# Performance work log

Measured on AMD Instinct MI355X. Metric: run time of the kernel, lower is better.

## Reference

```python
import jax, jax.numpy as jnp
import numpy as np

IN_F = 4096
OUT_F = 4096
B, S = 4, 2048
BITS = 4
N_LEVELS = 1 << BITS  # 16


def setup_inputs() -> dict:
    key = jax.random.key(0)
    kx, kr, ks, kb = jax.random.split(key, 4)
    x = jax.random.normal(kx, (B, S, IN_F), dtype=jnp.float32)
    # random orthogonal rotation (TurboQuantMSE rotation matrix, seeded)
    g = jax.random.normal(kr, (IN_F, IN_F), dtype=jnp.float32)
    rotation, _ = jnp.linalg.qr(g)
    # 4-bit scalar codebook: Lloyd-Max-style Gaussian levels, scaled for
    # unit-norm rows whose rotated entries ~ N(0, 1/in_features)
    p = (jnp.arange(N_LEVELS, dtype=jnp.float32) + 0.5) / N_LEVELS
    levels = jnp.sqrt(2.0) * jax.scipy.special.erfinv(2.0 * p - 1.0)
    codebook = (levels / jnp.sqrt(jnp.float32(IN_F))).astype(jnp.float32)
    weight_indices = jax.random.randint(jax.random.fold_in(key, 1), (OUT_F, IN_F), 0, N_LEVELS, dtype=jnp.int32)
    weight_scale = jax.random.uniform(ks, (OUT_F,), dtype=jnp.float32, minval=0.5, maxval=2.0)
    bias = jax.random.normal(kb, (OUT_F,), dtype=jnp.float32)
    return {"x": x, "weight_indices": weight_indices, "weight_scale": weight_scale,
            "bias": bias, "rotation": rotation, "codebook": codebook}


def reference(x, weight_indices, weight_scale, bias, rotation, codebook):
    # dequantize: codebook lookup -> inverse rotation -> per-row rescale
    w_rot = codebook[weight_indices]                      # (out, in)
    w_hat = jnp.einsum('oi,ji->oj', w_rot, rotation)      # apply R^T: (out, in)
    w = w_hat * weight_scale[:, None]                     # (out, in)
    # F.linear: x @ W^T + b
    return jnp.einsum('bsi,oi->bso', x, w) + bias
```

## Files before the change

kernel.cpp:

```cpp
#include <hip/hip_runtime.h>

typedef short short8 __attribute__((ext_vector_type(8)));
typedef float f32x4 __attribute__((ext_vector_type(4)));

#define GLOBAL_AS __attribute__((address_space(1)))
#define LDS_AS    __attribute__((address_space(3)))

__device__ __forceinline__ unsigned short f2bf(float f) {
    unsigned u = __builtin_bit_cast(unsigned, f);
    u += 0x7fffu + ((u >> 16) & 1u);
    return (unsigned short)(u >> 16);
}

__global__ __launch_bounds__(256) void k_idx2bf(const int* __restrict__ idx,
                                                const float* __restrict__ cb,
                                                ushort* __restrict__ out, int n4) {
    int i = blockIdx.x * 256 + threadIdx.x;
    if (i >= n4) return;
    int4 v = reinterpret_cast<const int4*>(idx)[i];
    ushort4 o;
    o.x = f2bf(cb[v.x]); o.y = f2bf(cb[v.y]);
    o.z = f2bf(cb[v.z]); o.w = f2bf(cb[v.w]);
    reinterpret_cast<ushort4*>(out)[i] = o;
}

__global__ __launch_bounds__(256) void k_f2bf(const float* __restrict__ in,
                                              ushort* __restrict__ out, int n4) {
    int i = blockIdx.x * 256 + threadIdx.x;
    if (i >= n4) return;
    float4 v = reinterpret_cast<const float4*>(in)[i];
    ushort4 o;
    o.x = f2bf(v.x); o.y = f2bf(v.y); o.z = f2bf(v.z); o.w = f2bf(v.w);
    reinterpret_cast<ushort4*>(out)[i] = o;
}


#define CH_AE(j) ((((j) & 8) << 1) | ((j) & 7))
#define CH_AL(j) (CH_AE(j) + 8)
#define CH_BE(j) ((((j) & 12) << 1) | ((j) & 3))
#define CH_BL(j) (CH_BE(j) + 4)

#define STAGE2(GB, LW, KB, CF) do {                                             \
    const int c0_ = CF(2 * w);                                                  \
    const int c1_ = CF(2 * w + 1);                                              \
    __builtin_amdgcn_global_load_lds(                                           \
        (const GLOBAL_AS void*)((GB) + (size_t)c0_ * 32768 + (KB)),             \
        (LDS_AS void*)((LW) + c0_ * 512), 16, 0, 0);                            \
    __builtin_amdgcn_global_load_lds(                                           \
        (const GLOBAL_AS void*)((GB) + (size_t)c1_ * 32768 + (KB)),             \
        (LDS_AS void*)((LW) + c1_ * 512), 16, 0, 0);                            \
} while (0)

#define READ_A(DST, BUF, MH) do {                                               \
    _Pragma("unroll")                                                           \
    for (int mi = 0; mi < 4; ++mi)                                              \
        DST[0][mi] = *reinterpret_cast<const short8*>(                          \
            sAc + ak0 + ((BUF) * 32768 + (MH) * 8192 + mi * 2048));             \
    _Pragma("unroll")                                                           \
    for (int mi = 0; mi < 4; ++mi)                                              \
        DST[1][mi] = *reinterpret_cast<const short8*>(                          \
            sAc + ak1 + ((BUF) * 32768 + (MH) * 8192 + mi * 2048));             \
} while (0)

#define READ_B(DST, BUF, NH) do {                                               \
    _Pragma("unroll")                                                           \
    for (int ni = 0; ni < 2; ++ni)                                              \
        DST[0][ni] = *reinterpret_cast<const short8*>(                          \
            sBc + bk0 + ((BUF) * 32768 + (NH) * 4096 + ni * 2048));             \
    _Pragma("unroll")                                                           \
    for (int ni = 0; ni < 2; ++ni)                                              \
        DST[1][ni] = *reinterpret_cast<const short8*>(                          \
            sBc + bk1 + ((BUF) * 32768 + (NH) * 4096 + ni * 2048));             \
} while (0)

#define MFMA16(MH, NH, AF, BF)                                                  \
    _Pragma("unroll")                                                           \
    for (int k2 = 0; k2 < 2; ++k2)                                              \
        _Pragma("unroll")                                                       \
        for (int mi = 0; mi < 4; ++mi)                                          \
            _Pragma("unroll")                                                   \
            for (int ni = 0; ni < 2; ++ni)                                      \
                acc[(MH) * 4 + mi][(NH) * 2 + ni] =                             \
                    __builtin_amdgcn_mfma_f32_16x16x32_bf16(                    \
                        AF[k2][mi], BF[k2][ni], acc[(MH) * 4 + mi][(NH) * 2 + ni], 0, 0, 0)

#define PH_MID do {                                                             \
    asm volatile("" ::: "memory");                                              \
    __builtin_amdgcn_s_barrier();                                               \
    asm volatile("s_waitcnt lgkmcnt(0)" ::: "memory");                          \
    __builtin_amdgcn_sched_barrier(0);                                          \
    __builtin_amdgcn_s_setprio(1);                                              \
} while (0)

#define PH_END do {                                                             \
    __builtin_amdgcn_s_setprio(0);                                              \
    asm volatile("" ::: "memory");                                              \
    __builtin_amdgcn_s_barrier();                                               \
    asm volatile("" ::: "memory");                                              \
} while (0)

#define PH1S(BUF, ...) do {                                                     \
    READ_A(aF, BUF, 0); READ_B(b0f, BUF, 0);                                    \
    __VA_ARGS__;                                                                \
    asm volatile("s_waitcnt lgkmcnt(8)" ::: "memory");                          \
    PH_MID; MFMA16(0, 0, aF, b0f); PH_END;                                      \
} while (0)

#define PH2S(BUF, ...) do {                                                     \
    READ_B(b1f, BUF, 1);                                                        \
    __VA_ARGS__;                                                                \
    PH_MID; MFMA16(0, 1, aF, b1f); PH_END;                                      \
} while (0)

#define PH3S(BUF, ...) do {                                                     \
    READ_A(aF, BUF, 1);                                                         \
    __VA_ARGS__;                                                                \
    PH_MID; MFMA16(1, 0, aF, b0f); PH_END;                                      \
} while (0)

#define PH4S(FN, ...) do {                                                      \
    __VA_ARGS__;                                                                \
    PH_MID; MFMA16(1, 1, aF, b1f);                                              \
    __builtin_amdgcn_s_setprio(0);                                              \
    asm volatile("s_waitcnt vmcnt(" #FN ")" ::: "memory");                      \
    __builtin_amdgcn_s_barrier();                                               \
    asm volatile("" ::: "memory");                                              \
} while (0)

#define PH4SNF(...) do {                                                        \
    __VA_ARGS__;                                                                \
    PH_MID; MFMA16(1, 1, aF, b1f); PH_END;                                      \
} while (0)

template <int EPI>
__global__ __launch_bounds__(512, 2) void gemm256(const ushort* __restrict__ A,
                                                  const ushort* __restrict__ B,
                                                  void* __restrict__ C,
                                                  const float* __restrict__ extra) {
    constexpr int K = 4096, N = 4096;
    __shared__ ushort sA[2][256 * 64];
    __shared__ ushort sB[2][256 * 64];

    const int tid  = threadIdx.x;
    const int w    = tid >> 6;
    const int lane = tid & 63;
    const int wm = w >> 2, wn = w & 3;

    const int nwg = gridDim.x;
    const int sw  = ((int)blockIdx.x & 7) * (nwg >> 3) + ((int)blockIdx.x >> 3);
    const int m0 = (sw >> 4) * 256;
    const int n0 = (sw & 15) * 256;

    const int srow8 = lane >> 3;
    const int scol  = (((lane & 7) ^ (lane >> 3)) * 8);
    const ushort* gAl = A + (size_t)m0 * K + srow8 * 4096 + scol;
    const ushort* gBl = B + (size_t)n0 * K + srow8 * 4096 + scol;

    const int fr   = lane & 15;
    const int fkb  = ((lane >> 4) & 3) * 16;
    const int swb  = (fr & 7) << 4;
    const int arow = wm * 128 + fr;
    const int brow = wn * 64 + fr;
    const char* sAc = (const char*)&sA[0][0];
    const char* sBc = (const char*)&sB[0][0];
    const int ak0 = (arow * 128 + 0  + fkb) ^ swb;
    const int ak1 = (arow * 128 + 64 + fkb) ^ swb;
    const int bk0 = (brow * 128 + 0  + fkb) ^ swb;
    const int bk1 = (brow * 128 + 64 + fkb) ^ swb;

    f32x4 acc[8][4];
#pragma unroll
    for (int i = 0; i < 8; ++i)
#pragma unroll
        for (int j = 0; j < 4; ++j) acc[i][j] = (f32x4){0.f, 0.f, 0.f, 0.f};

    short8 aF[2][4], b0f[2][2], b1f[2][2];

    STAGE2(gAl, sA[0], 0, CH_AE); STAGE2(gBl, sB[0], 0, CH_BE);
    STAGE2(gBl, sB[0], 0, CH_BL); STAGE2(gAl, sA[0], 0, CH_AL);
    STAGE2(gAl, sA[1], 64, CH_AE); STAGE2(gBl, sB[1], 64, CH_BE);
    STAGE2(gBl, sB[1], 64, CH_BL);
    asm volatile("s_waitcnt vmcnt(6)" ::: "memory");
    __builtin_amdgcn_s_barrier();
    asm volatile("" ::: "memory");

    for (int pr = 0; pr < 31; ++pr) {
        const int t = 2 * pr;
        const int kb1 = (t + 1) * 64, kb2 = (t + 2) * 64, kb3 = (t + 3) * 64;
        PH1S(0, STAGE2(gAl, sA[1], kb1, CH_AL));
        PH2S(0, STAGE2(gAl, sA[0], kb2, CH_AE));
        PH3S(0, STAGE2(gBl, sB[0], kb2, CH_BE));
        PH4S(6, STAGE2(gBl, sB[0], kb2, CH_BL));
        PH1S(1, STAGE2(gAl, sA[0], kb2, CH_AL));
        PH2S(1, STAGE2(gAl, sA[1], kb3, CH_AE));
        PH3S(1, STAGE2(gBl, sB[1], kb3, CH_BE));
        PH4S(6, STAGE2(gBl, sB[1], kb3, CH_BL));
    }
    {
        PH1S(0, STAGE2(gAl, sA[1], 63 * 64, CH_AL));
        PH2S(0, ((void)0));
        PH3S(0, ((void)0));
        PH4S(0, ((void)0));
        PH1S(1, ((void)0));
        PH2S(1, ((void)0));
        PH3S(1, ((void)0));
        PH4SNF(((void)0));
    }

    const int rb = m0 + wm * 128 + ((lane >> 4) * 4);
    const int cb = n0 + wn * 64 + (lane & 15);
    if (EPI == 0) {
        ushort* Cw = (ushort*)C;
#pragma unroll
        for (int mi = 0; mi < 8; ++mi) {
#pragma unroll
            for (int r = 0; r < 4; ++r) {
                const int row = rb + mi * 16 + r;
                const float s = extra[row];
#pragma unroll
                for (int ni = 0; ni < 4; ++ni)
                    Cw[(size_t)row * N + cb + ni * 16] = f2bf(acc[mi][ni][r] * s);
            }
        }
    } else {
        float* Cf = (float*)C;
#pragma unroll
        for (int ni = 0; ni < 4; ++ni) {
            const float b = extra[cb + ni * 16];
#pragma unroll
            for (int mi = 0; mi < 8; ++mi) {
#pragma unroll
                for (int r = 0; r < 4; ++r) {
                    const int row = rb + mi * 16 + r;
                    Cf[(size_t)row * N + cb + ni * 16] = acc[mi][ni][r] + b;
                }
            }
        }
    }
}

extern "C" void kernel_launch(void* const* d_in, const int* in_sizes, int n_in,
                              void* d_out, int out_size, void* d_ws, size_t ws_size,
                              hipStream_t stream) {
    const float* x     = (const float*)d_in[0];
    const int*   widx  = (const int*)  d_in[1];
    const float* wscal = (const float*)d_in[2];
    const float* bias  = (const float*)d_in[3];
    const float* rot   = (const float*)d_in[4];
    const float* cb    = (const float*)d_in[5];
    float* out = (float*)d_out;

    constexpr size_t IN_F = 4096, OUT_F = 4096, MTOK = 8192;
    char* ws = (char*)d_ws;
    ushort* wq   = (ushort*)(ws);
    ushort* rbuf = (ushort*)(ws + 33554432);
    ushort* xb   = (ushort*)(ws + 67108864);
    ushort* wb   = (ushort*)(ws + 134217728);
    (void)ws_size; (void)in_sizes; (void)n_in; (void)out_size;

    {
        int n4 = (int)(OUT_F * IN_F / 4);
        k_idx2bf<<<n4 / 256, 256, 0, stream>>>(widx, cb, wq, n4);
        k_f2bf<<<n4 / 256, 256, 0, stream>>>(rot, rbuf, n4);
        int n4x = (int)(MTOK * IN_F / 4);
        k_f2bf<<<n4x / 256, 256, 0, stream>>>(x, xb, n4x);
    }

    gemm256<0><<<dim3(256), 512, 0, stream>>>(wq, rbuf, (void*)wb, wscal);

    gemm256<1><<<dim3(512), 512, 0, stream>>>(xb, wb, (void*)out, bias);
}
```

Before: 453.8 us.

## Software-pipeline LDS fragment reads one phase ahead of MFMA compute

```diff
diff --git a/kernel.cpp b/kernel.cpp
--- a/kernel.cpp
+++ b/kernel.cpp
@@ -55,22 +55,22 @@
     _Pragma("unroll")                                                           \
     for (int mi = 0; mi < 4; ++mi)                                              \
         DST[0][mi] = *reinterpret_cast<const short8*>(                          \
-            sAc + ak0 + ((BUF) * 32768 + (MH) * 8192 + mi * 2048));             \
+            aB0 + ((BUF) * 32768 + (MH) * 8192 + mi * 2048));                   \
     _Pragma("unroll")                                                           \
     for (int mi = 0; mi < 4; ++mi)                                              \
         DST[1][mi] = *reinterpret_cast<const short8*>(                          \
-            sAc + ak1 + ((BUF) * 32768 + (MH) * 8192 + mi * 2048));             \
+            aB1 + ((BUF) * 32768 + (MH) * 8192 + mi * 2048));                   \
 } while (0)
 
 #define READ_B(DST, BUF, NH) do {                                               \
     _Pragma("unroll")                                                           \
     for (int ni = 0; ni < 2; ++ni)                                              \
         DST[0][ni] = *reinterpret_cast<const short8*>(                          \
-            sBc + bk0 + ((BUF) * 32768 + (NH) * 4096 + ni * 2048));             \
+            bB0 + ((BUF) * 32768 + (NH) * 4096 + ni * 2048));                   \
     _Pragma("unroll")                                                           \
     for (int ni = 0; ni < 2; ++ni)                                              \
         DST[1][ni] = *reinterpret_cast<const short8*>(                          \
-            sBc + bk1 + ((BUF) * 32768 + (NH) * 4096 + ni * 2048));             \
+            bB1 + ((BUF) * 32768 + (NH) * 4096 + ni * 2048));                   \
 } while (0)
 
 #define MFMA16(MH, NH, AF, BF)                                                  \
@@ -84,10 +84,13 @@
                     __builtin_amdgcn_mfma_f32_16x16x32_bf16(                    \
                         AF[k2][mi], BF[k2][ni], acc[(MH) * 4 + mi][(NH) * 2 + ni], 0, 0, 0)
 
-#define PH_MID do {                                                             \
-    asm volatile("" ::: "memory");                                              \
-    __builtin_amdgcn_s_barrier();                                               \
-    asm volatile("s_waitcnt lgkmcnt(0)" ::: "memory");                          \
+#define PHTOP do {                                                              \
+    asm volatile("" ::: "memory");                                              \
+    __builtin_amdgcn_s_barrier();                                               \
+} while (0)
+
+#define PHMIDN(N) do {                                                          \
+    asm volatile("s_waitcnt lgkmcnt(" #N ")" ::: "memory");                     \
     __builtin_amdgcn_sched_barrier(0);                                          \
     __builtin_amdgcn_s_setprio(1);                                              \
 } while (0)
@@ -99,37 +102,50 @@
     asm volatile("" ::: "memory");                                              \
 } while (0)
 
-#define PH1S(BUF, ...) do {                                                     \
-    READ_A(aF, BUF, 0); READ_B(b0f, BUF, 0);                                    \
-    __VA_ARGS__;                                                                \
-    asm volatile("s_waitcnt lgkmcnt(8)" ::: "memory");                          \
-    PH_MID; MFMA16(0, 0, aF, b0f); PH_END;                                      \
-} while (0)
-
-#define PH2S(BUF, ...) do {                                                     \
+#define PH1N(BUF, ...) do {                                                     \
     READ_B(b1f, BUF, 1);                                                        \
     __VA_ARGS__;                                                                \
-    PH_MID; MFMA16(0, 1, aF, b1f); PH_END;                                      \
-} while (0)
-
-#define PH3S(BUF, ...) do {                                                     \
+    PHTOP; PHMIDN(4); MFMA16(0, 0, aF, b0f); PH_END;                            \
+} while (0)
+
+#define PH2N(BUF, ...) do {                                                     \
+    __VA_ARGS__;                                                                \
+    PHTOP; PHMIDN(0); MFMA16(0, 1, aF, b1f);                                    \
+    __builtin_amdgcn_s_setprio(0);                                              \
     READ_A(aF, BUF, 1);                                                         \
-    __VA_ARGS__;                                                                \
-    PH_MID; MFMA16(1, 0, aF, b0f); PH_END;                                      \
-} while (0)
-
-#define PH4S(FN, ...) do {                                                      \
-    __VA_ARGS__;                                                                \
-    PH_MID; MFMA16(1, 1, aF, b1f);                                              \
+    asm volatile("" ::: "memory");                                              \
+    __builtin_amdgcn_s_barrier();                                               \
+    asm volatile("" ::: "memory");                                              \
+} while (0)
+
+#define PH3N(FN, ...) do {                                                      \
+    __VA_ARGS__;                                                                \
+    PHTOP; PHMIDN(0); MFMA16(1, 0, aF, b0f);                                    \
     __builtin_amdgcn_s_setprio(0);                                              \
     asm volatile("s_waitcnt vmcnt(" #FN ")" ::: "memory");                      \
     __builtin_amdgcn_s_barrier();                                               \
     asm volatile("" ::: "memory");                                              \
 } while (0)
 
-#define PH4SNF(...) do {                                                        \
-    __VA_ARGS__;                                                                \
-    PH_MID; MFMA16(1, 1, aF, b1f); PH_END;                                      \
+#define PH3T(...) do {                                                          \
+    __VA_ARGS__;                                                                \
+    PHTOP; PHMIDN(0); MFMA16(1, 0, aF, b0f); PH_END;                            \
+} while (0)
+
+#define PH4N(NBUF, FN, ...) do {                                                \
+    READ_B(b0f, NBUF, 0);                                                       \
+    __VA_ARGS__;                                                                \
+    PHTOP; PHMIDN(4); MFMA16(1, 1, aF, b1f);                                    \
+    __builtin_amdgcn_s_setprio(0);                                              \
+    READ_A(aF, NBUF, 0);                                                        \
+    asm volatile("s_waitcnt vmcnt(" #FN ")" ::: "memory");                      \
+    __builtin_amdgcn_s_barrier();                                               \
+    asm volatile("" ::: "memory");                                              \
+} while (0)
+
+#define PH4T(...) do {                                                          \
+    __VA_ARGS__;                                                                \
+    PHTOP; PHMIDN(0); MFMA16(1, 1, aF, b1f); PH_END;                            \
 } while (0)
 
 template <int EPI>
@@ -161,12 +177,10 @@
     const int swb  = (fr & 7) << 4;
     const int arow = wm * 128 + fr;
     const int brow = wn * 64 + fr;
-    const char* sAc = (const char*)&sA[0][0];
-    const char* sBc = (const char*)&sB[0][0];
-    const int ak0 = (arow * 128 + 0  + fkb) ^ swb;
-    const int ak1 = (arow * 128 + 64 + fkb) ^ swb;
-    const int bk0 = (brow * 128 + 0  + fkb) ^ swb;
-    const int bk1 = (brow * 128 + 64 + fkb) ^ swb;
+    const char* aB0 = (const char*)&sA[0][0] + ((arow * 128 + 0  + fkb) ^ swb);
+    const char* aB1 = (const char*)&sA[0][0] + ((arow * 128 + 64 + fkb) ^ swb);
+    const char* bB0 = (const char*)&sB[0][0] + ((brow * 128 + 0  + fkb) ^ swb);
+    const char* bB1 = (const char*)&sB[0][0] + ((brow * 128 + 64 + fkb) ^ swb);
 
     f32x4 acc[8][4];
 #pragma unroll
@@ -183,28 +197,29 @@
     asm volatile("s_waitcnt vmcnt(6)" ::: "memory");
     __builtin_amdgcn_s_barrier();
     asm volatile("" ::: "memory");
+    READ_A(aF, 0, 0); READ_B(b0f, 0, 0);
 
     for (int pr = 0; pr < 31; ++pr) {
         const int t = 2 * pr;
         const int kb1 = (t + 1) * 64, kb2 = (t + 2) * 64, kb3 = (t + 3) * 64;
-        PH1S(0, STAGE2(gAl, sA[1], kb1, CH_AL));
-        PH2S(0, STAGE2(gAl, sA[0], kb2, CH_AE));
-        PH3S(0, STAGE2(gBl, sB[0], kb2, CH_BE));
-        PH4S(6, STAGE2(gBl, sB[0], kb2, CH_BL));
-        PH1S(1, STAGE2(gAl, sA[0], kb2, CH_AL));
-        PH2S(1, STAGE2(gAl, sA[1], kb3, CH_AE));
-        PH3S(1, STAGE2(gBl, sB[1], kb3, CH_BE));
-        PH4S(6, STAGE2(gBl, sB[1], kb3, CH_BL));
+        PH1N(0,    STAGE2(gAl, sA[1], kb1, CH_AL));
+        PH2N(0,    STAGE2(gAl, sA[0], kb2, CH_AE));
+        PH3N(8,    STAGE2(gBl, sB[0], kb2, CH_BE));
+        PH4N(1, 6, STAGE2(gBl, sB[0], kb2, CH_BL));
+        PH1N(1,    STAGE2(gAl, sA[0], kb2, CH_AL));
+        PH2N(1,    STAGE2(gAl, sA[1], kb3, CH_AE));
+        PH3N(8,    STAGE2(gBl, sB[1], kb3, CH_BE));
+        PH4N(0, 6, STAGE2(gBl, sB[1], kb3, CH_BL));
     }
     {
-        PH1S(0, STAGE2(gAl, sA[1], 63 * 64, CH_AL));
-        PH2S(0, ((void)0));
-        PH3S(0, ((void)0));
-        PH4S(0, ((void)0));
-        PH1S(1, ((void)0));
-        PH2S(1, ((void)0));
-        PH3S(1, ((void)0));
-        PH4SNF(((void)0));
+        PH1N(0,    STAGE2(gAl, sA[1], 63 * 64, CH_AL));
+        PH2N(0,    ((void)0));
+        PH3N(4,    ((void)0));
+        PH4N(1, 0, ((void)0));
+        PH1N(1,    ((void)0));
+        PH2N(1,    ((void)0));
+        PH3T(((void)0));
+        PH4T(((void)0));
     }
 
     const int rb = m0 + wm * 128 + ((lane >> 4) * 4);
```

Measured after the change: 482.7 us. 1.06x slower.

## Merge four GEMM phases per K-tile into two with split lgkmcnt waits

Applied to the files above, without the earlier changes.

```diff
diff --git a/kernel.cpp b/kernel.cpp
--- a/kernel.cpp
+++ b/kernel.cpp
@@ -73,7 +73,7 @@
             sBc + bk1 + ((BUF) * 32768 + (NH) * 4096 + ni * 2048));             \
 } while (0)
 
-#define MFMA16(MH, NH, AF, BF)                                                  \
+#define MFMA16(MH, NH, BF)                                                      \
     _Pragma("unroll")                                                           \
     for (int k2 = 0; k2 < 2; ++k2)                                              \
         _Pragma("unroll")                                                       \
@@ -82,54 +82,66 @@
             for (int ni = 0; ni < 2; ++ni)                                      \
                 acc[(MH) * 4 + mi][(NH) * 2 + ni] =                             \
                     __builtin_amdgcn_mfma_f32_16x16x32_bf16(                    \
-                        AF[k2][mi], BF[k2][ni], acc[(MH) * 4 + mi][(NH) * 2 + ni], 0, 0, 0)
-
-#define PH_MID do {                                                             \
-    asm volatile("" ::: "memory");                                              \
-    __builtin_amdgcn_s_barrier();                                               \
-    asm volatile("s_waitcnt lgkmcnt(0)" ::: "memory");                          \
+                        aF[k2][mi], BF[k2][ni], acc[(MH) * 4 + mi][(NH) * 2 + ni], 0, 0, 0)
+
+#define MFMA8K(MH, NH, K2, BF)                                                  \
+    _Pragma("unroll")                                                           \
+    for (int mi = 0; mi < 4; ++mi)                                              \
+        _Pragma("unroll")                                                       \
+        for (int ni = 0; ni < 2; ++ni)                                          \
+            acc[(MH) * 4 + mi][(NH) * 2 + ni] =                                 \
+                __builtin_amdgcn_mfma_f32_16x16x32_bf16(                        \
+                    aF[K2][mi], BF[K2][ni], acc[(MH) * 4 + mi][(NH) * 2 + ni], 0, 0, 0)
+
+#define LG(N) do {                                                              \
+    asm volatile("s_waitcnt lgkmcnt(" #N ")" ::: "memory");                     \
     __builtin_amdgcn_sched_barrier(0);                                          \
-    __builtin_amdgcn_s_setprio(1);                                              \
-} while (0)
-
-#define PH_END do {                                                             \
-    __builtin_amdgcn_s_setprio(0);                                              \
+} while (0)
+
+#define BAR do {                                                                \
     asm volatile("" ::: "memory");                                              \
     __builtin_amdgcn_s_barrier();                                               \
     asm volatile("" ::: "memory");                                              \
 } while (0)
 
-#define PH1S(BUF, ...) do {                                                     \
-    READ_A(aF, BUF, 0); READ_B(b0f, BUF, 0);                                    \
+#define PH1M(BUF, ...) do {                                                     \
+    READ_B(b0f, BUF, 0); READ_A(aF, BUF, 0); READ_B(b1f, BUF, 1);               \
     __VA_ARGS__;                                                                \
-    asm volatile("s_waitcnt lgkmcnt(8)" ::: "memory");                          \
-    PH_MID; MFMA16(0, 0, aF, b0f); PH_END;                                      \
-} while (0)
-
-#define PH2S(BUF, ...) do {                                                     \
-    READ_B(b1f, BUF, 1);                                                        \
-    __VA_ARGS__;                                                                \
-    PH_MID; MFMA16(0, 1, aF, b1f); PH_END;                                      \
-} while (0)
-
-#define PH3S(BUF, ...) do {                                                     \
+    BAR;                                                                        \
+    LG(4); __builtin_amdgcn_s_setprio(1);                                       \
+    MFMA16(0, 0, b0f);                                                          \
+    LG(0);                                                                      \
+    MFMA16(0, 1, b1f);                                                          \
+    __builtin_amdgcn_s_setprio(0);                                              \
+    BAR;                                                                        \
+} while (0)
+
+#define PH2M(BUF, FN, ...) do {                                                 \
     READ_A(aF, BUF, 1);                                                         \
     __VA_ARGS__;                                                                \
-    PH_MID; MFMA16(1, 0, aF, b0f); PH_END;                                      \
-} while (0)
-
-#define PH4S(FN, ...) do {                                                      \
-    __VA_ARGS__;                                                                \
-    PH_MID; MFMA16(1, 1, aF, b1f);                                              \
+    BAR;                                                                        \
+    LG(4); __builtin_amdgcn_s_setprio(1);                                       \
+    MFMA8K(1, 0, 0, b0f);                                                       \
+    LG(0);                                                                      \
+    MFMA8K(1, 0, 1, b0f);                                                       \
+    MFMA16(1, 1, b1f);                                                          \
     __builtin_amdgcn_s_setprio(0);                                              \
     asm volatile("s_waitcnt vmcnt(" #FN ")" ::: "memory");                      \
     __builtin_amdgcn_s_barrier();                                               \
     asm volatile("" ::: "memory");                                              \
 } while (0)
 
-#define PH4SNF(...) do {                                                        \
+#define PH2MNF(BUF, ...) do {                                                   \
+    READ_A(aF, BUF, 1);                                                         \
     __VA_ARGS__;                                                                \
-    PH_MID; MFMA16(1, 1, aF, b1f); PH_END;                                      \
+    BAR;                                                                        \
+    LG(4); __builtin_amdgcn_s_setprio(1);                                       \
+    MFMA8K(1, 0, 0, b0f);                                                       \
+    LG(0);                                                                      \
+    MFMA8K(1, 0, 1, b0f);                                                       \
+    MFMA16(1, 1, b1f);                                                          \
+    __builtin_amdgcn_s_setprio(0);                                              \
+    BAR;                                                                        \
 } while (0)
 
 template <int EPI>
@@ -177,34 +189,25 @@
     short8 aF[2][4], b0f[2][2], b1f[2][2];
 
     STAGE2(gAl, sA[0], 0, CH_AE); STAGE2(gBl, sB[0], 0, CH_BE);
-    STAGE2(gBl, sB[0], 0, CH_BL); STAGE2(gAl, sA[0], 0, CH_AL);
+    STAGE2(gAl, sA[0], 0, CH_AL); STAGE2(gBl, sB[0], 0, CH_BL);
     STAGE2(gAl, sA[1], 64, CH_AE); STAGE2(gBl, sB[1], 64, CH_BE);
-    STAGE2(gBl, sB[1], 64, CH_BL);
-    asm volatile("s_waitcnt vmcnt(6)" ::: "memory");
+    asm volatile("s_waitcnt vmcnt(4)" ::: "memory");
     __builtin_amdgcn_s_barrier();
     asm volatile("" ::: "memory");
 
     for (int pr = 0; pr < 31; ++pr) {
         const int t = 2 * pr;
         const int kb1 = (t + 1) * 64, kb2 = (t + 2) * 64, kb3 = (t + 3) * 64;
-        PH1S(0, STAGE2(gAl, sA[1], kb1, CH_AL));
-        PH2S(0, STAGE2(gAl, sA[0], kb2, CH_AE));
-        PH3S(0, STAGE2(gBl, sB[0], kb2, CH_BE));
-        PH4S(6, STAGE2(gBl, sB[0], kb2, CH_BL));
-        PH1S(1, STAGE2(gAl, sA[0], kb2, CH_AL));
-        PH2S(1, STAGE2(gAl, sA[1], kb3, CH_AE));
-        PH3S(1, STAGE2(gBl, sB[1], kb3, CH_BE));
-        PH4S(6, STAGE2(gBl, sB[1], kb3, CH_BL));
+        PH1M(0,    STAGE2(gAl, sA[1], kb1, CH_AL); STAGE2(gBl, sB[1], kb1, CH_BL));
+        PH2M(0, 4, STAGE2(gAl, sA[0], kb2, CH_AE); STAGE2(gBl, sB[0], kb2, CH_BE));
+        PH1M(1,    STAGE2(gAl, sA[0], kb2, CH_AL); STAGE2(gBl, sB[0], kb2, CH_BL));
+        PH2M(1, 4, STAGE2(gAl, sA[1], kb3, CH_AE); STAGE2(gBl, sB[1], kb3, CH_BE));
     }
     {
-        PH1S(0, STAGE2(gAl, sA[1], 63 * 64, CH_AL));
-        PH2S(0, ((void)0));
-        PH3S(0, ((void)0));
-        PH4S(0, ((void)0));
-        PH1S(1, ((void)0));
-        PH2S(1, ((void)0));
-        PH3S(1, ((void)0));
-        PH4SNF(((void)0));
+        PH1M(0,    STAGE2(gAl, sA[1], 63 * 64, CH_AL); STAGE2(gBl, sB[1], 63 * 64, CH_BL));
+        PH2M(0, 0, ((void)0));
+        PH1M(1, ((void)0));
+        PH2MNF(1, ((void)0));
     }
 
     const int rb = m0 + wm * 128 + ((lane >> 4) * 4);
```

Result: slower. 472.2 us (+4.1%).

## Restructure GEMM phase pipeline to prefetch B fragments and drop lgkmcnt waits

Applied to the files above, without the earlier changes.

```diff
diff --git a/kernel.cpp b/kernel.cpp
--- a/kernel.cpp
+++ b/kernel.cpp
@@ -55,25 +55,25 @@
     _Pragma("unroll")                                                           \
     for (int mi = 0; mi < 4; ++mi)                                              \
         DST[0][mi] = *reinterpret_cast<const short8*>(                          \
-            sAc + ak0 + ((BUF) * 32768 + (MH) * 8192 + mi * 2048));             \
+            sAc + ak0 + ((BUF) + (MH) * 8192 + mi * 2048));                     \
     _Pragma("unroll")                                                           \
     for (int mi = 0; mi < 4; ++mi)                                              \
         DST[1][mi] = *reinterpret_cast<const short8*>(                          \
-            sAc + ak1 + ((BUF) * 32768 + (MH) * 8192 + mi * 2048));             \
+            sAc + ak1 + ((BUF) + (MH) * 8192 + mi * 2048));                     \
 } while (0)
 
 #define READ_B(DST, BUF, NH) do {                                               \
     _Pragma("unroll")                                                           \
     for (int ni = 0; ni < 2; ++ni)                                              \
         DST[0][ni] = *reinterpret_cast<const short8*>(                          \
-            sBc + bk0 + ((BUF) * 32768 + (NH) * 4096 + ni * 2048));             \
+            sBc + bk0 + ((BUF) + (NH) * 4096 + ni * 2048));                     \
     _Pragma("unroll")                                                           \
     for (int ni = 0; ni < 2; ++ni)                                              \
         DST[1][ni] = *reinterpret_cast<const short8*>(                          \
-            sBc + bk1 + ((BUF) * 32768 + (NH) * 4096 + ni * 2048));             \
-} while (0)
-
-#define MFMA16(MH, NH, AF, BF)                                                  \
+            sBc + bk1 + ((BUF) + (NH) * 4096 + ni * 2048));                     \
+} while (0)
+
+#define MFMA16Q(MH, NH, AF, BF)                                                 \
     _Pragma("unroll")                                                           \
     for (int k2 = 0; k2 < 2; ++k2)                                              \
         _Pragma("unroll")                                                       \
@@ -84,52 +84,67 @@
                     __builtin_amdgcn_mfma_f32_16x16x32_bf16(                    \
                         AF[k2][mi], BF[k2][ni], acc[(MH) * 4 + mi][(NH) * 2 + ni], 0, 0, 0)
 
-#define PH_MID do {                                                             \
+#define PH_BAR do {                                                             \
     asm volatile("" ::: "memory");                                              \
     __builtin_amdgcn_s_barrier();                                               \
-    asm volatile("s_waitcnt lgkmcnt(0)" ::: "memory");                          \
-    __builtin_amdgcn_sched_barrier(0);                                          \
-    __builtin_amdgcn_s_setprio(1);                                              \
-} while (0)
-
-#define PH_END do {                                                             \
-    __builtin_amdgcn_s_setprio(0);                                              \
-    asm volatile("" ::: "memory");                                              \
-    __builtin_amdgcn_s_barrier();                                               \
-    asm volatile("" ::: "memory");                                              \
-} while (0)
-
-#define PH1S(BUF, ...) do {                                                     \
-    READ_A(aF, BUF, 0); READ_B(b0f, BUF, 0);                                    \
-    __VA_ARGS__;                                                                \
-    asm volatile("s_waitcnt lgkmcnt(8)" ::: "memory");                          \
-    PH_MID; MFMA16(0, 0, aF, b0f); PH_END;                                      \
-} while (0)
-
-#define PH2S(BUF, ...) do {                                                     \
+    asm volatile("" ::: "memory");                                              \
+} while (0)
+
+#define PH1R(BUF, ...) do {                                                     \
+    READ_A(aF, BUF, 0);                                                         \
+    __VA_ARGS__;                                                                \
+    PH_BAR;                                                                     \
+    __builtin_amdgcn_s_setprio(1); MFMA16Q(0, 0, aF, b0f);                      \
+    __builtin_amdgcn_s_setprio(0);                                              \
+    PH_BAR;                                                                     \
+} while (0)
+
+#define PH2R(BUF, ...) do {                                                     \
     READ_B(b1f, BUF, 1);                                                        \
     __VA_ARGS__;                                                                \
-    PH_MID; MFMA16(0, 1, aF, b1f); PH_END;                                      \
-} while (0)
-
-#define PH3S(BUF, ...) do {                                                     \
+    PH_BAR;                                                                     \
+    __builtin_amdgcn_s_setprio(1); MFMA16Q(0, 1, aF, b1f);                      \
+    __builtin_amdgcn_s_setprio(0);                                              \
+    PH_BAR;                                                                     \
+} while (0)
+
+#define PH3R(BUF, FN, ...) do {                                                 \
     READ_A(aF, BUF, 1);                                                         \
     __VA_ARGS__;                                                                \
-    PH_MID; MFMA16(1, 0, aF, b0f); PH_END;                                      \
-} while (0)
-
-#define PH4S(FN, ...) do {                                                      \
-    __VA_ARGS__;                                                                \
-    PH_MID; MFMA16(1, 1, aF, b1f);                                              \
+    PH_BAR;                                                                     \
+    __builtin_amdgcn_s_setprio(1); MFMA16Q(1, 0, aF, b0f);                      \
     __builtin_amdgcn_s_setprio(0);                                              \
     asm volatile("s_waitcnt vmcnt(" #FN ")" ::: "memory");                      \
     __builtin_amdgcn_s_barrier();                                               \
     asm volatile("" ::: "memory");                                              \
 } while (0)
 
-#define PH4SNF(...) do {                                                        \
-    __VA_ARGS__;                                                                \
-    PH_MID; MFMA16(1, 1, aF, b1f); PH_END;                                      \
+#define PH3RNF(BUF, ...) do {                                                   \
+    READ_A(aF, BUF, 1);                                                         \
+    __VA_ARGS__;                                                                \
+    PH_BAR;                                                                     \
+    __builtin_amdgcn_s_setprio(1); MFMA16Q(1, 0, aF, b0f);                      \
+    __builtin_amdgcn_s_setprio(0);                                              \
+    PH_BAR;                                                                     \
+} while (0)
+
+#define PH4R(NBUF, FN, ...) do {                                                \
+    READ_B(b0f, NBUF, 0);                                                       \
+    __VA_ARGS__;                                                                \
+    PH_BAR;                                                                     \
+    __builtin_amdgcn_s_setprio(1); MFMA16Q(1, 1, aF, b1f);                      \
+    __builtin_amdgcn_s_setprio(0);                                              \
+    asm volatile("s_waitcnt vmcnt(" #FN ")" ::: "memory");                      \
+    __builtin_amdgcn_s_barrier();                                               \
+    asm volatile("" ::: "memory");                                              \
+} while (0)
+
+#define PH4RNF(...) do {                                                        \
+    __VA_ARGS__;                                                                \
+    PH_BAR;                                                                     \
+    __builtin_amdgcn_s_setprio(1); MFMA16Q(1, 1, aF, b1f);                      \
+    __builtin_amdgcn_s_setprio(0);                                              \
+    PH_BAR;                                                                     \
 } while (0)
 
 template <int EPI>
@@ -183,28 +198,29 @@
     asm volatile("s_waitcnt vmcnt(6)" ::: "memory");
     __builtin_amdgcn_s_barrier();
     asm volatile("" ::: "memory");
+    READ_B(b0f, 0, 0);
 
     for (int pr = 0; pr < 31; ++pr) {
         const int t = 2 * pr;
         const int kb1 = (t + 1) * 64, kb2 = (t + 2) * 64, kb3 = (t + 3) * 64;
-        PH1S(0, STAGE2(gAl, sA[1], kb1, CH_AL));
-        PH2S(0, STAGE2(gAl, sA[0], kb2, CH_AE));
-        PH3S(0, STAGE2(gBl, sB[0], kb2, CH_BE));
-        PH4S(6, STAGE2(gBl, sB[0], kb2, CH_BL));
-        PH1S(1, STAGE2(gAl, sA[0], kb2, CH_AL));
-        PH2S(1, STAGE2(gAl, sA[1], kb3, CH_AE));
-        PH3S(1, STAGE2(gBl, sB[1], kb3, CH_BE));
-        PH4S(6, STAGE2(gBl, sB[1], kb3, CH_BL));
+        PH1R(0,        STAGE2(gAl, sA[1], kb1, CH_AL));
+        PH2R(0,        STAGE2(gAl, sA[0], kb2, CH_AE));
+        PH3R(0, 6,     STAGE2(gBl, sB[0], kb2, CH_BE));
+        PH4R(32768, 6, STAGE2(gBl, sB[0], kb2, CH_BL));
+        PH1R(32768,    STAGE2(gAl, sA[0], kb2, CH_AL));
+        PH2R(32768,    STAGE2(gAl, sA[1], kb3, CH_AE));
+        PH3R(32768, 6, STAGE2(gBl, sB[1], kb3, CH_BE));
+        PH4R(0, 6,     STAGE2(gBl, sB[1], kb3, CH_BL));
     }
     {
-        PH1S(0, STAGE2(gAl, sA[1], 63 * 64, CH_AL));
-        PH2S(0, ((void)0));
-        PH3S(0, ((void)0));
-        PH4S(0, ((void)0));
-        PH1S(1, ((void)0));
-        PH2S(1, ((void)0));
-        PH3S(1, ((void)0));
-        PH4SNF(((void)0));
+        PH1R(0,        STAGE2(gAl, sA[1], 63 * 64, CH_AL));
+        PH2R(0,        ((void)0));
+        PH3R(0, 2,     ((void)0));
+        PH4R(32768, 0, ((void)0));
+        PH1R(32768,    ((void)0));
+        PH2R(32768,    ((void)0));
+        PH3RNF(32768,  ((void)0));
+        PH4RNF(((void)0));
     }
 
     const int rb = m0 + wm * 128 + ((lane >> 4) * 4);
```

Measured after the change: 479.6 us. 5.7% more time.
